# Kernel tuning notes

Measured on AMD Instinct MI355X. Metric: run time of the kernel, lower is better.

Reference implementation:

```python
import jax, jax.numpy as jnp
import numpy as np


def setup_inputs() -> dict:
    key = jax.random.key(0)
    k1, k2, k3, k4 = jax.random.split(key, 4)
    N, E, D = 100000, 1250000, 64
    return {
        "src_embedding": jax.random.normal(k1, (N, D), dtype=jnp.float32),
        "edge_embedding": jax.random.normal(k2, (E, D), dtype=jnp.float32),
        "src_idx": jax.random.randint(k3, (E,), 0, N, dtype=jnp.int64),
        "dst_idx": jax.random.randint(k4, (E,), 0, N, dtype=jnp.int64),
        "num_nodes": N,
    }


def reference(src_embedding, edge_embedding, src_idx, dst_idx, num_nodes):
    # message: msg = h_src + h_edge  (gather on src, elementwise add)
    msg = src_embedding[src_idx] + edge_embedding  # [E, D]
    # reduce: per-destination mean over incoming edges (segment mean)
    agg_sum = jax.ops.segment_sum(msg, dst_idx, num_segments=num_nodes)  # [N, D]
    deg = jax.ops.segment_sum(jnp.ones_like(dst_idx, dtype=msg.dtype), dst_idx,
                              num_segments=num_nodes)  # [N]
    # nodes with no incoming edges get zeros (DGL leaves them zero-initialized)
    return agg_sum / jnp.maximum(deg, 1.0)[:, None]
```

## Files before the change

### kernel.cpp

```cpp
#include <hip/hip_runtime.h>


#define D 64
#define SCAN_BLK 1024

__global__ __launch_bounds__(256) void hist_kernel(
    const int* __restrict__ dst_idx, int* __restrict__ counts, int E)
{
    int e = blockIdx.x * blockDim.x + threadIdx.x;
    if (e < E) atomicAdd(counts + dst_idx[e], 1);
}

__global__ __launch_bounds__(256) void scan_partial_kernel(
    const int* __restrict__ counts, int* __restrict__ blockSums, int N)
{
    __shared__ int red[256];
    const int t = threadIdx.x, b = blockIdx.x;
    const int base = b * SCAN_BLK + t * 4;
    int s = 0;
    #pragma unroll
    for (int k = 0; k < 4; ++k) { int i = base + k; if (i < N) s += counts[i]; }
    red[t] = s; __syncthreads();
    for (int off = 128; off; off >>= 1) {
        if (t < off) red[t] += red[t + off];
        __syncthreads();
    }
    if (t == 0) blockSums[b] = red[0];
}

__global__ __launch_bounds__(1024) void scan_sums_kernel(
    const int* __restrict__ blockSums, int* __restrict__ blockBase,
    int numBlocks, int* __restrict__ offsets, int N)
{
    __shared__ int s[1024];
    const int t = threadIdx.x;
    int v = (t < numBlocks) ? blockSums[t] : 0;
    s[t] = v; __syncthreads();
    for (int off = 1; off < 1024; off <<= 1) {
        int u = (t >= off) ? s[t - off] : 0;
        __syncthreads();
        if (t >= off) s[t] += u;
        __syncthreads();
    }
    if (t < numBlocks) blockBase[t] = (t == 0) ? 0 : s[t - 1];
    if (t == numBlocks - 1) offsets[N] = s[t];
}

__global__ __launch_bounds__(256) void scan_final_kernel(
    const int* __restrict__ counts, const int* __restrict__ blockBase,
    int* __restrict__ offsets, int* __restrict__ cursor, int N)
{
    __shared__ int sc[256];
    const int t = threadIdx.x, b = blockIdx.x;
    const int base = b * SCAN_BLK + t * 4;
    int local[4];
    int s = 0;
    #pragma unroll
    for (int k = 0; k < 4; ++k) {
        int i = base + k;
        int c = (i < N) ? counts[i] : 0;
        local[k] = s; s += c;
    }
    sc[t] = s; __syncthreads();
    for (int off = 1; off < 256; off <<= 1) {
        int u = (t >= off) ? sc[t - off] : 0;
        __syncthreads();
        if (t >= off) sc[t] += u;
        __syncthreads();
    }
    const int thrBase = blockBase[b] + ((t == 0) ? 0 : sc[t - 1]);
    #pragma unroll
    for (int k = 0; k < 4; ++k) {
        int i = base + k;
        if (i < N) { int v = thrBase + local[k]; offsets[i] = v; cursor[i] = v; }
    }
}

__global__ __launch_bounds__(256) void pair_scatter_kernel(
    const int* __restrict__ src_idx,
    const int* __restrict__ dst_idx,
    int*       __restrict__ cursor,
    int2*      __restrict__ pairs,
    int E)
{
    int e = blockIdx.x * blockDim.x + threadIdx.x;
    if (e >= E) return;
    int pos = atomicAdd(cursor + dst_idx[e], 1);
    pairs[pos] = make_int2(e, src_idx[e]);
}

__global__ __launch_bounds__(256) void reduce_kernel(
    const float* __restrict__ src_emb,
    const float* __restrict__ edge_emb,
    const int2*  __restrict__ pairs,
    const int*   __restrict__ offsets,
    float*       __restrict__ out,
    int N)
{
    const int wave = (blockIdx.x * blockDim.x + threadIdx.x) >> 6;
    const int lane = threadIdx.x & 63;
    if (wave >= N) return;

    const int beg = offsets[wave];
    const int end = offsets[wave + 1];

    float acc = 0.0f;

    for (int base = beg; base < end; base += 64) {
        const int cnt = min(64, end - base);
        int2 pr = make_int2(0, 0);
        if (lane < cnt) pr = pairs[base + lane];

        int j = 0;
        for (; j + 1 < cnt; j += 2) {
            const int e0 = __builtin_amdgcn_readlane(pr.x, j);
            const int s0 = __builtin_amdgcn_readlane(pr.y, j);
            const int e1 = __builtin_amdgcn_readlane(pr.x, j + 1);
            const int s1 = __builtin_amdgcn_readlane(pr.y, j + 1);
            const float v0 = edge_emb[(size_t)e0 * D + lane];
            const float v1 = src_emb [(size_t)s0 * D + lane];
            const float v2 = edge_emb[(size_t)e1 * D + lane];
            const float v3 = src_emb [(size_t)s1 * D + lane];
            acc += (v0 + v1) + (v2 + v3);
        }
        if (j < cnt) {
            const int e0 = __builtin_amdgcn_readlane(pr.x, j);
            const int s0 = __builtin_amdgcn_readlane(pr.y, j);
            acc += edge_emb[(size_t)e0 * D + lane] + src_emb[(size_t)s0 * D + lane];
        }
    }

    const int deg = end - beg;
    const float inv = (deg > 0) ? (1.0f / (float)deg) : 0.0f;
    out[(size_t)wave * D + lane] = acc * inv;
}

extern "C" void kernel_launch(void* const* d_in, const int* in_sizes, int n_in,
                              void* d_out, int out_size, void* d_ws, size_t ws_size,
                              hipStream_t stream) {
    const float* src_emb  = (const float*)d_in[0];
    const float* edge_emb = (const float*)d_in[1];
    const int*   src_idx  = (const int*)d_in[2];
    const int*   dst_idx  = (const int*)d_in[3];

    const int E = in_sizes[2];
    const int N = out_size / D;

    float* out = (float*)d_out;

    int* wsi       = (int*)d_ws;
    int* offsets   = wsi;
    int* counts    = offsets + (N + 1);
    int* cursor    = counts + N;
    int* blockSums = cursor + N;
    int* blockBase = blockSums + 1024;
    size_t hdr = (size_t)(N + 1) + N + N + 1024 + 1024;
    hdr = (hdr + 1) & ~(size_t)1;
    int2* pairs = (int2*)(wsi + hdr);

    const int numBlocks = (N + SCAN_BLK - 1) / SCAN_BLK;

    (void)hipMemsetAsync(counts, 0, (size_t)N * sizeof(int), stream);
    hist_kernel<<<(E + 255) / 256, 256, 0, stream>>>(dst_idx, counts, E);
    scan_partial_kernel<<<numBlocks, 256, 0, stream>>>(counts, blockSums, N);
    scan_sums_kernel<<<1, 1024, 0, stream>>>(blockSums, blockBase, numBlocks, offsets, N);
    scan_final_kernel<<<numBlocks, 256, 0, stream>>>(counts, blockBase, offsets, cursor, N);

    pair_scatter_kernel<<<(E + 255) / 256, 256, 0, stream>>>(src_idx, dst_idx,
                                                             cursor, pairs, E);
    {
        int grid = (N + 3) / 4;
        reduce_kernel<<<grid, 256, 0, stream>>>(src_emb, edge_emb, pairs,
                                                offsets, out, N);
    }
}
```

Before: 624.8 us.

## Record histogram ranks to drop scatter atomics; vectorize reduce with 4 edges per wave

The histogram kernel now stores each edge's atomic return value as its rank, so the pair scatter computes its slot as offsets[dst]+rank with no second atomic pass and no cursor array. The reduce kernel now splits each wave into four 16-lane groups, each loading float4 slices of a different edge row, with nontemporal loads for edge embeddings. Partial sums are combined with xor shuffles and written out as vectorized nontemporal stores. This trades an extra E-sized rank buffer (written then read) for fewer atomics and more memory-level parallelism in the gather.

```diff
diff --git a/kernel.cpp b/kernel.cpp
--- a/kernel.cpp
+++ b/kernel.cpp
@@ -4,11 +4,14 @@
 #define D 64
 #define SCAN_BLK 1024
 
+typedef float f32x4 __attribute__((ext_vector_type(4)));
+
 __global__ __launch_bounds__(256) void hist_kernel(
-    const int* __restrict__ dst_idx, int* __restrict__ counts, int E)
+    const int* __restrict__ dst_idx, int* __restrict__ counts,
+    int* __restrict__ rank, int E)
 {
     int e = blockIdx.x * blockDim.x + threadIdx.x;
-    if (e < E) atomicAdd(counts + dst_idx[e], 1);
+    if (e < E) rank[e] = atomicAdd(counts + dst_idx[e], 1);
 }
 
 __global__ __launch_bounds__(256) void scan_partial_kernel(
@@ -48,7 +51,7 @@
 
 __global__ __launch_bounds__(256) void scan_final_kernel(
     const int* __restrict__ counts, const int* __restrict__ blockBase,
-    int* __restrict__ offsets, int* __restrict__ cursor, int N)
+    int* __restrict__ offsets, int N)
 {
     __shared__ int sc[256];
     const int t = threadIdx.x, b = blockIdx.x;
@@ -72,20 +75,21 @@
     #pragma unroll
     for (int k = 0; k < 4; ++k) {
         int i = base + k;
-        if (i < N) { int v = thrBase + local[k]; offsets[i] = v; cursor[i] = v; }
+        if (i < N) offsets[i] = thrBase + local[k];
     }
 }
 
 __global__ __launch_bounds__(256) void pair_scatter_kernel(
     const int* __restrict__ src_idx,
     const int* __restrict__ dst_idx,
-    int*       __restrict__ cursor,
+    const int* __restrict__ rank,
+    const int* __restrict__ offsets,
     int2*      __restrict__ pairs,
     int E)
 {
     int e = blockIdx.x * blockDim.x + threadIdx.x;
     if (e >= E) return;
-    int pos = atomicAdd(cursor + dst_idx[e], 1);
+    int pos = offsets[dst_idx[e]] + rank[e];
     pairs[pos] = make_int2(e, src_idx[e]);
 }
 
@@ -103,36 +107,57 @@
 
     const int beg = offsets[wave];
     const int end = offsets[wave + 1];
-
-    float acc = 0.0f;
+    const int grp = lane >> 4;
+    const int cg  = (lane & 15) << 2;
+
+    f32x4 acc = {0.f, 0.f, 0.f, 0.f};
 
     for (int base = beg; base < end; base += 64) {
-        const int cnt = min(64, end - base);
+        const int cnt  = min(64, end - base);
+        const int last = cnt - 1;
         int2 pr = make_int2(0, 0);
         if (lane < cnt) pr = pairs[base + lane];
 
-        int j = 0;
-        for (; j + 1 < cnt; j += 2) {
-            const int e0 = __builtin_amdgcn_readlane(pr.x, j);
-            const int s0 = __builtin_amdgcn_readlane(pr.y, j);
-            const int e1 = __builtin_amdgcn_readlane(pr.x, j + 1);
-            const int s1 = __builtin_amdgcn_readlane(pr.y, j + 1);
-            const float v0 = edge_emb[(size_t)e0 * D + lane];
-            const float v1 = src_emb [(size_t)s0 * D + lane];
-            const float v2 = edge_emb[(size_t)e1 * D + lane];
-            const float v3 = src_emb [(size_t)s1 * D + lane];
-            acc += (v0 + v1) + (v2 + v3);
+        for (int j = 0; j < cnt; j += 8) {
+            const int i0 = j + grp;
+            const int i1 = i0 + 4;
+            const bool v0 = (i0 <= last);
+            const bool v1 = (i1 <= last);
+            const int k0 = v0 ? i0 : last;
+            const int k1 = v1 ? i1 : last;
+            const int e0 = __shfl(pr.x, k0);
+            const int s0 = __shfl(pr.y, k0);
+            const int e1 = __shfl(pr.x, k1);
+            const int s1 = __shfl(pr.y, k1);
+
+            f32x4 ev0 = __builtin_nontemporal_load(
+                (const f32x4*)(edge_emb + ((size_t)e0 << 6) + cg));
+            f32x4 sv0 = *(const f32x4*)(src_emb + ((size_t)s0 << 6) + cg);
+            f32x4 ev1 = __builtin_nontemporal_load(
+                (const f32x4*)(edge_emb + ((size_t)e1 << 6) + cg));
+            f32x4 sv1 = *(const f32x4*)(src_emb + ((size_t)s1 << 6) + cg);
+
+            f32x4 z = {0.f, 0.f, 0.f, 0.f};
+            acc += v0 ? (ev0 + sv0) : z;
+            acc += v1 ? (ev1 + sv1) : z;
         }
-        if (j < cnt) {
-            const int e0 = __builtin_amdgcn_readlane(pr.x, j);
-            const int s0 = __builtin_amdgcn_readlane(pr.y, j);
-            acc += edge_emb[(size_t)e0 * D + lane] + src_emb[(size_t)s0 * D + lane];
-        }
-    }
+    }
+
+    acc.x += __shfl_xor(acc.x, 16);
+    acc.y += __shfl_xor(acc.y, 16);
+    acc.z += __shfl_xor(acc.z, 16);
+    acc.w += __shfl_xor(acc.w, 16);
+    acc.x += __shfl_xor(acc.x, 32);
+    acc.y += __shfl_xor(acc.y, 32);
+    acc.z += __shfl_xor(acc.z, 32);
+    acc.w += __shfl_xor(acc.w, 32);
 
     const int deg = end - beg;
     const float inv = (deg > 0) ? (1.0f / (float)deg) : 0.0f;
-    out[(size_t)wave * D + lane] = acc * inv;
+    if (grp == 0) {
+        f32x4 r = acc * inv;
+        __builtin_nontemporal_store(r, (f32x4*)(out + ((size_t)wave << 6) + cg));
+    }
 }
 
 extern "C" void kernel_launch(void* const* d_in, const int* in_sizes, int n_in,
@@ -151,23 +176,23 @@
     int* wsi       = (int*)d_ws;
     int* offsets   = wsi;
     int* counts    = offsets + (N + 1);
-    int* cursor    = counts + N;
-    int* blockSums = cursor + N;
+    int* rank      = counts + N;
+    int* blockSums = rank + E;
     int* blockBase = blockSums + 1024;
-    size_t hdr = (size_t)(N + 1) + N + N + 1024 + 1024;
+    size_t hdr = (size_t)(N + 1) + N + E + 1024 + 1024;
     hdr = (hdr + 1) & ~(size_t)1;
     int2* pairs = (int2*)(wsi + hdr);
 
     const int numBlocks = (N + SCAN_BLK - 1) / SCAN_BLK;
 
     (void)hipMemsetAsync(counts, 0, (size_t)N * sizeof(int), stream);
-    hist_kernel<<<(E + 255) / 256, 256, 0, stream>>>(dst_idx, counts, E);
+    hist_kernel<<<(E + 255) / 256, 256, 0, stream>>>(dst_idx, counts, rank, E);
     scan_partial_kernel<<<numBlocks, 256, 0, stream>>>(counts, blockSums, N);
     scan_sums_kernel<<<1, 1024, 0, stream>>>(blockSums, blockBase, numBlocks, offsets, N);
-    scan_final_kernel<<<numBlocks, 256, 0, stream>>>(counts, blockBase, offsets, cursor, N);
+    scan_final_kernel<<<numBlocks, 256, 0, stream>>>(counts, blockBase, offsets, N);
 
     pair_scatter_kernel<<<(E + 255) / 256, 256, 0, stream>>>(src_idx, dst_idx,
-                                                             cursor, pairs, E);
+                                                             rank, offsets, pairs, E);
     {
         int grid = (N + 3) / 4;
         reduce_kernel<<<grid, 256, 0, stream>>>(src_emb, edge_emb, pairs,
```

Measured after the change: 549.7 us. 1.14x faster.
